# Kernel tuning notes

Measured on AMD Instinct MI355X. Metric: run time of the kernel, lower is better.

Reference implementation:

```python
import jax, jax.numpy as jnp
import numpy as np

N = 50000        # nodes
E = 500000       # edges
NUM = 4          # sampled intermediate neighbors per edge (self.num)
F = 64           # in_feats == out_feats (transform=False)
D = 32           # dist_dim
NB = 64          # embedding rows = len(boundaries)+1


def setup_inputs() -> dict:
    key = jax.random.key(0)
    ks = jax.random.split(key, 10)
    feat = jax.random.normal(ks[0], (N, F), jnp.float32)
    loc = jax.random.uniform(ks[1], (N, 3), jnp.float32)          # 3D positions in unit cube
    boundaries = jnp.sort(jax.random.uniform(ks[2], (NB - 1,), jnp.float32, 0.0, 2.0))
    embed_table = jax.random.normal(ks[3], (NB, D), jnp.float32)
    G_w = jax.random.normal(ks[4], (F, D), jnp.float32) / np.sqrt(D)      # Linear(dist_dim->out, no bias)
    agg_w = jax.random.normal(ks[5], (F, 2 * F), jnp.float32) / np.sqrt(2 * F)  # Linear(2*out->out)
    agg_b = jnp.zeros((F,), jnp.float32)
    src = jax.random.randint(ks[6], (E,), 0, N, jnp.int32)
    dst = jax.random.randint(ks[7], (E,), 0, N, jnp.int32)
    inter_ids = jax.random.randint(ks[8], (E, NUM), 0, N, jnp.int32)
    return dict(feat=feat, loc=loc, boundaries=boundaries, embed_table=embed_table,
                G_w=G_w, agg_w=agg_w, agg_b=agg_b, src=src, dst=dst, inter_ids=inter_ids)


def reference(feat, loc, boundaries, embed_table, G_w, agg_w, agg_b, src, dst, inter_ids):
    n = feat.shape[0]
    ones = jnp.ones((src.shape[0],), feat.dtype)
    # symmetric-ish degree normalization: d0 = in_deg^-0.5, d2 = out_deg^-0.5
    in_deg = jax.ops.segment_sum(ones, dst, num_segments=n)
    out_deg = jax.ops.segment_sum(ones, src, num_segments=n)
    d0 = jnp.clip(in_deg, 1.0) ** -0.5   # [N]
    d2 = jnp.clip(out_deg, 1.0) ** -0.5  # [N]

    # dist1 = ||loc[dst] - loc[src]||_2, bucketize -> embed -> G
    dist1 = jnp.linalg.norm(loc[dst] - loc[src], axis=1)              # [E]
    de1 = embed_table[jnp.searchsorted(boundaries, dist1)] @ G_w.T    # [E, F]

    # intermediate sampled neighbors: dist to each sampled node from edge src
    pos_src = loc[src]                                                # [E, 3]
    inter_pos = loc[inter_ids]                                        # [E, NUM, 3]
    dist_ = jnp.linalg.norm(pos_src[:, None, :] - inter_pos, axis=-1) # [E, NUM]
    de_ = embed_table[jnp.searchsorted(boundaries, dist_)] @ G_w.T    # [E, NUM, F]
    inter_h = feat[inter_ids]                                         # [E, NUM, F]
    dist_embed_dot_h = (de_ * inter_h).mean(axis=1)                   # [E, F]

    # h = d0[dst] * d2[src] * agg_fc([de1 * h_src, dist_embed_dot_h])
    cat = jnp.concatenate([de1 * feat[src], dist_embed_dot_h], axis=1)  # [E, 2F]
    msg = (d0[dst] * d2[src])[:, None] * (cat @ agg_w.T + agg_b)        # [E, F]

    # update_all(copy_e('h'), sum) -> scatter-sum messages to dst
    ft = jax.ops.segment_sum(msg, dst, num_segments=n)                  # [N, F]
    return ft
```

## Files before the change

### kernel.cpp

```cpp
#include <hip/hip_runtime.h>
#include <math.h>

#define LUTN 1024
#define LUTSCALE 512.0f
#define NBINS 50048
#define CHSH 12


__global__ __launch_bounds__(256) void prep_kernel(
    const float* __restrict__ embed, const float* __restrict__ G_w,
    const float* __restrict__ boundaries, const float* __restrict__ feat,
    const float* __restrict__ loc,
    float* __restrict__ M, int* __restrict__ lut,
    unsigned short* __restrict__ featH, float4* __restrict__ loc4, int N) {

    const int gid = blockIdx.x * 256 + threadIdx.x;
    const int gsz = gridDim.x * 256;
    for (int i = gid; i < 4096; i += gsz) {
        int b = i >> 6, f = i & 63;
        float acc = 0.f;
        #pragma unroll
        for (int dd = 0; dd < 32; ++dd) acc += embed[b * 32 + dd] * G_w[f * 32 + dd];
        M[i] = acc;
    }
    for (int i = gid; i < LUTN; i += gsz) {
        float left = (float)i * (1.0f / LUTSCALE);
        int c = 0;
        for (int j = 0; j < 63; ++j) c += (boundaries[j] < left) ? 1 : 0;
        lut[i] = c;
    }
    const int nq = N * 16;
    for (int i = gid; i < nq; i += gsz) {
        float4 v = ((const float4*)feat)[i];
        unsigned ux = __float_as_uint(v.x), uy = __float_as_uint(v.y);
        unsigned uz = __float_as_uint(v.z), uw = __float_as_uint(v.w);
        ushort4 h;
        h.x = (unsigned short)((ux + 0x7FFFu + ((ux >> 16) & 1u)) >> 16);
        h.y = (unsigned short)((uy + 0x7FFFu + ((uy >> 16) & 1u)) >> 16);
        h.z = (unsigned short)((uz + 0x7FFFu + ((uz >> 16) & 1u)) >> 16);
        h.w = (unsigned short)((uw + 0x7FFFu + ((uw >> 16) & 1u)) >> 16);
        ((ushort4*)featH)[i] = h;
    }
    for (int i = gid; i < N; i += gsz)
        loc4[i] = make_float4(loc[3 * i], loc[3 * i + 1], loc[3 * i + 2], 0.f);
}


__global__ __launch_bounds__(256) void hist_kernel(
    const int* __restrict__ src, const int* __restrict__ dst,
    unsigned char* __restrict__ pcnt, unsigned char* __restrict__ psrc,
    unsigned char* __restrict__ rnk8, int E) {

    __shared__ unsigned int hc[NBINS / 4];
    __shared__ unsigned int hs[NBINS / 4];
    for (int i = threadIdx.x; i < NBINS / 4; i += 256) { hc[i] = 0u; hs[i] = 0u; }
    __syncthreads();

    const int base = blockIdx.x << CHSH;
    const int lim  = min(E - base, 1 << CHSH);
    for (int t = threadIdx.x; t < lim; t += 256) {
        const int e = base + t;
        const int d = dst[e];
        const int s = src[e];
        const unsigned sh = (unsigned)(d & 3) * 8u;
        unsigned old = atomicAdd(&hc[d >> 2], 1u << sh);
        rnk8[e] = (unsigned char)((old >> sh) & 0xFFu);
        atomicAdd(&hs[s >> 2], 1u << ((unsigned)(s & 3) * 8u));
    }
    __syncthreads();

    unsigned int* gc = (unsigned int*)(pcnt + (size_t)blockIdx.x * NBINS);
    unsigned int* gs = (unsigned int*)(psrc + (size_t)blockIdx.x * NBINS);
    for (int i = threadIdx.x; i < NBINS / 4; i += 256) { gc[i] = hc[i]; gs[i] = hs[i]; }
}


__global__ __launch_bounds__(256) void merge_kernel(
    unsigned char* __restrict__ pcnt, const unsigned char* __restrict__ psrc,
    int* __restrict__ cnt, float* __restrict__ d2w, int P, int N) {

    const int d = blockIdx.x * 256 + threadIdx.x;
    if (d >= N) return;

    int sc = 0;
    #pragma unroll 4
    for (int p = 0; p < P; ++p) {
        const size_t idx = (size_t)p * NBINS + d;
        const int c = pcnt[idx];
        pcnt[idx] = (unsigned char)sc;
        sc += c;
    }
    cnt[d] = sc;

    int ss = 0;
    #pragma unroll 4
    for (int p = 0; p < P; ++p) ss += psrc[(size_t)p * NBINS + d];
    d2w[d] = rsqrtf(fmaxf((float)ss, 1.0f));
}


__global__ __launch_bounds__(1024) void scan_block_kernel(
    const int* __restrict__ cnt, int* __restrict__ startv,
    int* __restrict__ part, int N) {

    __shared__ int wsum[16];
    const int t = threadIdx.x, lane = t & 63, wv = t >> 6;
    const int i = blockIdx.x * 1024 + t;

    int v = (i < N) ? cnt[i] : 0;
    int x = v;
    #pragma unroll
    for (int off = 1; off < 64; off <<= 1) { int y = __shfl_up(x, off); if (lane >= off) x += y; }
    if (lane == 63) wsum[wv] = x;
    __syncthreads();
    if (t < 16) {
        int w = wsum[t], xx = w;
        #pragma unroll
        for (int off = 1; off < 16; off <<= 1) { int y = __shfl_up(xx, off); if (t >= off) xx += y; }
        wsum[t] = xx - w;
    }
    __syncthreads();
    int incl = x + wsum[wv];
    if (i < N) startv[i] = incl - v;
    if (t == 1023) part[blockIdx.x] = incl;
}

__device__ __forceinline__ void load_chunkoff(const int* __restrict__ part, int nb,
                                              int* __restrict__ co) {
    if (threadIdx.x < 64) {
        int v = (threadIdx.x < nb) ? part[threadIdx.x] : 0;
        int x = v;
        #pragma unroll
        for (int off = 1; off < 64; off <<= 1) {
            int y = __shfl_up(x, off);
            if ((threadIdx.x & 63) >= off) x += y;
        }
        co[threadIdx.x] = x - v;
    }
    __syncthreads();
}


__global__ __launch_bounds__(256) void edge_kernel(
    const float4* __restrict__ loc4, const float* __restrict__ boundaries,
    const int* __restrict__ lut,
    const int* __restrict__ src, const int* __restrict__ dst,
    const int* __restrict__ inter,
    const unsigned char* __restrict__ rnk8, const unsigned char* __restrict__ pcnt,
    const int* __restrict__ startv, const int* __restrict__ part,
    const float* __restrict__ d2w,
    int4* __restrict__ rec, int E, int nb) {

    __shared__ int lut_s[LUTN];
    __shared__ float bl[64];
    __shared__ int co[64];
    ((int4*)lut_s)[threadIdx.x] = ((const int4*)lut)[threadIdx.x];
    if (threadIdx.x < 64)
        bl[threadIdx.x] = (threadIdx.x < 63) ? boundaries[threadIdx.x] : 3.4e38f;
    load_chunkoff(part, nb, co);

    const int e = blockIdx.x * 256 + threadIdx.x;
    if (e >= E) return;

    const int s = src[e], d = dst[e];
    const int4 ii = ((const int4*)inter)[e];

    const float4 ps = loc4[s];
    float dist[5];
    {
        float4 pd = loc4[d];
        float dx = pd.x - ps.x, dy = pd.y - ps.y, dz = pd.z - ps.z;
        dist[0] = sqrtf(dx * dx + dy * dy + dz * dz);
    }
    const int id4[4] = {ii.x, ii.y, ii.z, ii.w};
    #pragma unroll
    for (int j = 0; j < 4; ++j) {
        float4 pt = loc4[id4[j]];
        float dx = pt.x - ps.x, dy = pt.y - ps.y, dz = pt.z - ps.z;
        dist[1 + j] = sqrtf(dx * dx + dy * dy + dz * dz);
    }
    unsigned pack = 0;
    #pragma unroll
    for (int q = 0; q < 5; ++q) {
        float dq = dist[q];
        int cell = (int)(dq * LUTSCALE);
        cell = (cell > LUTN - 1) ? (LUTN - 1) : cell;
        int b = lut_s[cell];
        while (b < 63 && bl[b] < dq) ++b;
        while (b > 0 && bl[b - 1] >= dq) --b;
        pack |= ((unsigned)b) << (6 * q);
    }

    const int p = e >> CHSH;
    const int cbase = pcnt[(size_t)p * NBINS + d];
    const int pos = startv[d] + co[d >> 10] + cbase + (int)rnk8[e];
    const float w = d2w[s];
    unsigned uw = __float_as_uint(w);
    unsigned wb = (uw + 0x7FFFu + ((uw >> 16) & 1u)) & 0xFFFF0000u;
    rec[pos] = make_int4(s | (ii.x << 16), ii.y | (ii.z << 16), ii.w | (int)wb, (int)pack);
}


__global__ __launch_bounds__(256) void node_kernel(
    const unsigned short* __restrict__ featH, const float* __restrict__ M,
    const int* __restrict__ cnt, const int* __restrict__ startv,
    const int* __restrict__ part, const int4* __restrict__ rec,
    float* __restrict__ cat, float* __restrict__ swb, int N, int nb) {

    __shared__ float Ms[4096];
    __shared__ int co[64];
    #pragma unroll
    for (int i = 0; i < 4; ++i)
        ((float4*)Ms)[threadIdx.x + 256 * i] = ((const float4*)M)[threadIdx.x + 256 * i];
    load_chunkoff(part, nb, co);

    const int lane = threadIdx.x & 63;
    const int wid  = threadIdx.x >> 6;
    const int d    = blockIdx.x * 4 + wid;
    if (d >= N) return;

    const int deg  = __builtin_amdgcn_readfirstlane(cnt[d]);
    const int base = __builtin_amdgcn_readfirstlane(startv[d] + co[d >> 10]);
    const int4* rp = rec + base;

    float acc0 = 0.f, acc1 = 0.f, sw = 0.f;

    #pragma unroll 4
    for (int k = 0; k < deg; ++k) {
        const int4 r = rp[k];
        const int s  = r.x & 0xFFFF;
        const int i0 = ((unsigned)r.x) >> 16;
        const int i1 = r.y & 0xFFFF;
        const int i2 = ((unsigned)r.y) >> 16;
        const int i3 = r.z & 0xFFFF;
        const float w = __uint_as_float((unsigned)r.z & 0xFFFF0000u);
        const unsigned pk = (unsigned)r.w;

        const float fs = __uint_as_float(((unsigned)featH[(size_t)s  * 64 + lane]) << 16);
        const float f0 = __uint_as_float(((unsigned)featH[(size_t)i0 * 64 + lane]) << 16);
        const float f1 = __uint_as_float(((unsigned)featH[(size_t)i1 * 64 + lane]) << 16);
        const float f2 = __uint_as_float(((unsigned)featH[(size_t)i2 * 64 + lane]) << 16);
        const float f3 = __uint_as_float(((unsigned)featH[(size_t)i3 * 64 + lane]) << 16);
        const float m0 = Ms[(pk & 63u) * 64 + lane];
        const float m1 = Ms[((pk >> 6) & 63u) * 64 + lane];
        const float m2 = Ms[((pk >> 12) & 63u) * 64 + lane];
        const float m3 = Ms[((pk >> 18) & 63u) * 64 + lane];
        const float m4 = Ms[((pk >> 24) & 63u) * 64 + lane];

        acc0 = fmaf(m0 * fs, w, acc0);
        float t = m1 * f0 + m2 * f1 + m3 * f2 + m4 * f3;
        acc1 = fmaf(0.25f * t, w, acc1);
        sw += w;
    }

    cat[(size_t)d * 128 + lane]      = acc0;
    cat[(size_t)d * 128 + 64 + lane] = acc1;
    if (lane == 0) swb[d] = sw;
}


__global__ __launch_bounds__(256) void epilogue_kernel(
    const float* __restrict__ cat, const float* __restrict__ agg_w,
    const float* __restrict__ agg_b, const float* __restrict__ swb,
    const int* __restrict__ cnt, float* __restrict__ out, int N) {

    const int lane = threadIdx.x & 63;
    const int wid  = threadIdx.x >> 6;

    float4 aw[32];
    const float4* awp = (const float4*)(agg_w + (size_t)lane * 128);
    #pragma unroll
    for (int i = 0; i < 32; ++i) aw[i] = awp[i];
    const float bias = agg_b[lane];

    const int gw = blockIdx.x * 4 + wid;
    const int stride = gridDim.x * 4;

    for (int d0i = gw; d0i < N; d0i += stride) {
        const int du = __builtin_amdgcn_readfirstlane(d0i);
        const float* cp = cat + (size_t)du * 128;
        float a0 = bias * swb[du], a1 = 0.f, a2 = 0.f, a3 = 0.f;
        #pragma unroll
        for (int k4 = 0; k4 < 32; k4 += 4) {
            float4 c0 = ((const float4*)cp)[k4];
            float4 c1 = ((const float4*)cp)[k4 + 1];
            float4 c2 = ((const float4*)cp)[k4 + 2];
            float4 c3 = ((const float4*)cp)[k4 + 3];
            a0 = fmaf(aw[k4].x, c0.x, a0); a0 = fmaf(aw[k4].y, c0.y, a0);
            a0 = fmaf(aw[k4].z, c0.z, a0); a0 = fmaf(aw[k4].w, c0.w, a0);
            a1 = fmaf(aw[k4+1].x, c1.x, a1); a1 = fmaf(aw[k4+1].y, c1.y, a1);
            a1 = fmaf(aw[k4+1].z, c1.z, a1); a1 = fmaf(aw[k4+1].w, c1.w, a1);
            a2 = fmaf(aw[k4+2].x, c2.x, a2); a2 = fmaf(aw[k4+2].y, c2.y, a2);
            a2 = fmaf(aw[k4+2].z, c2.z, a2); a2 = fmaf(aw[k4+2].w, c2.w, a2);
            a3 = fmaf(aw[k4+3].x, c3.x, a3); a3 = fmaf(aw[k4+3].y, c3.y, a3);
            a3 = fmaf(aw[k4+3].z, c3.z, a3); a3 = fmaf(aw[k4+3].w, c3.w, a3);
        }
        const float d0v = rsqrtf(fmaxf((float)cnt[du], 1.0f));
        out[(size_t)du * 64 + lane] = d0v * ((a0 + a1) + (a2 + a3));
    }
}


extern "C" void kernel_launch(void* const* d_in, const int* in_sizes, int n_in,
                              void* d_out, int out_size, void* d_ws, size_t ws_size,
                              hipStream_t stream) {
    const float* feat       = (const float*)d_in[0];
    const float* loc        = (const float*)d_in[1];
    const float* boundaries = (const float*)d_in[2];
    const float* embed      = (const float*)d_in[3];
    const float* G_w        = (const float*)d_in[4];
    const float* agg_w      = (const float*)d_in[5];
    const float* agg_b      = (const float*)d_in[6];
    const int*   src        = (const int*)d_in[7];
    const int*   dst        = (const int*)d_in[8];
    const int*   inter      = (const int*)d_in[9];

    const int N = in_sizes[0] / 64;
    const int E = in_sizes[7];

    const int P = (E + (1 << CHSH) - 1) >> CHSH;

    char* w = (char*)d_ws;
    auto take = [&](size_t bytes) { char* p = w; w += (bytes + 15) & ~(size_t)15; return p; };
    float*          M      = (float*)take(4096 * 4);
    int*            lut    = (int*)  take(LUTN * 4);
    int*            cnt    = (int*)  take((size_t)N * 4);
    int*            startv = (int*)  take((size_t)N * 4);
    int*            part   = (int*)  take(64 * 4);
    float*          d2w    = (float*)take((size_t)N * 4);
    int4*           rec    = (int4*) take((size_t)E * 16);
    unsigned char*  rnk8   = (unsigned char*)take((size_t)E);
    unsigned char*  pcnt   = (unsigned char*)take((size_t)P * NBINS);
    unsigned char*  psrc   = (unsigned char*)take((size_t)P * NBINS);
    float*          cat    = (float*)take((size_t)N * 128 * 4);
    float*          swb    = (float*)take((size_t)N * 4);
    unsigned short* featH  = (unsigned short*)take((size_t)N * 64 * 2);
    float4*         loc4   = (float4*)take((size_t)N * 16);
    float*          out    = (float*)d_out;

    const int eb = (E + 255) / 256;
    const int nb = (N + 1023) / 1024;
    const int mb = (N + 255) / 256;

    prep_kernel<<<1024, 256, 0, stream>>>(embed, G_w, boundaries, feat, loc,
                                          M, lut, featH, loc4, N);
    hist_kernel<<<P, 256, 0, stream>>>(src, dst, pcnt, psrc, rnk8, E);
    merge_kernel<<<mb, 256, 0, stream>>>(pcnt, psrc, cnt, d2w, P, N);
    scan_block_kernel<<<nb, 1024, 0, stream>>>(cnt, startv, part, N);
    edge_kernel<<<eb, 256, 0, stream>>>(loc4, boundaries, lut, src, dst, inter,
                                        rnk8, pcnt, startv, part, d2w, rec, E, nb);
    node_kernel<<<(N + 3) / 4, 256, 0, stream>>>(featH, M, cnt, startv, part, rec,
                                                 cat, swb, N, nb);
    epilogue_kernel<<<768, 256, 0, stream>>>(cat, agg_w, agg_b, swb, cnt, out, N);
}
```

Measured before the change: 232.9 us.

## Fuse prep/histogram and merge/scan kernels; split node gather across half-waves

The prep and histogram kernels become one launch, with histogram blocks and prep blocks running side by side. The histogram now reuses a single shared buffer for the dst and src passes, halving LDS so more blocks fit per CU. The merge and block-scan kernels are fused so counts feed the scan directly, removing a launch and a round trip of cnt. The node kernel now has each half-wave process alternate edges with 2-wide bf16 loads, then combines the halves with a cross-lane shuffle. This trades extra passes over src/dst and lower occupancy in merge_scan (1024-thread blocks) for fewer launches and more memory-level parallelism.

Measured after the change: 238.0 us. 2.2% more time.

```diff
diff --git a/kernel.cpp b/kernel.cpp
--- a/kernel.cpp
+++ b/kernel.cpp
@@ -4,18 +4,55 @@
 #define LUTN 1024
 #define LUTSCALE 512.0f
 #define NBINS 50048
+#define HCW (NBINS / 4)
 #define CHSH 12
 
 
-__global__ __launch_bounds__(256) void prep_kernel(
+__global__ __launch_bounds__(256) void front_kernel(
     const float* __restrict__ embed, const float* __restrict__ G_w,
     const float* __restrict__ boundaries, const float* __restrict__ feat,
     const float* __restrict__ loc,
+    const int* __restrict__ src, const int* __restrict__ dst,
     float* __restrict__ M, int* __restrict__ lut,
-    unsigned short* __restrict__ featH, float4* __restrict__ loc4, int N) {
-
-    const int gid = blockIdx.x * 256 + threadIdx.x;
-    const int gsz = gridDim.x * 256;
+    unsigned short* __restrict__ featH, float4* __restrict__ loc4,
+    unsigned char* __restrict__ pcnt, unsigned char* __restrict__ psrc,
+    unsigned char* __restrict__ rnk8,
+    int N, int E, int P, int PREPB) {
+
+    __shared__ unsigned int h[HCW];
+
+    if (blockIdx.x < P) {
+        const int base = blockIdx.x << CHSH;
+        const int lim  = min(E - base, 1 << CHSH);
+
+        for (int i = threadIdx.x; i < HCW; i += 256) h[i] = 0u;
+        __syncthreads();
+        for (int t = threadIdx.x; t < lim; t += 256) {
+            const int e = base + t;
+            const int dd = dst[e];
+            const unsigned sh = (unsigned)(dd & 3) * 8u;
+            unsigned old = atomicAdd(&h[dd >> 2], 1u << sh);
+            rnk8[e] = (unsigned char)((old >> sh) & 0xFFu);
+        }
+        __syncthreads();
+        unsigned int* gc = (unsigned int*)(pcnt + (size_t)blockIdx.x * NBINS);
+        for (int i = threadIdx.x; i < HCW; i += 256) gc[i] = h[i];
+        __syncthreads();
+
+        for (int i = threadIdx.x; i < HCW; i += 256) h[i] = 0u;
+        __syncthreads();
+        for (int t = threadIdx.x; t < lim; t += 256) {
+            const int s = src[base + t];
+            atomicAdd(&h[s >> 2], 1u << ((unsigned)(s & 3) * 8u));
+        }
+        __syncthreads();
+        unsigned int* gs = (unsigned int*)(psrc + (size_t)blockIdx.x * NBINS);
+        for (int i = threadIdx.x; i < HCW; i += 256) gs[i] = h[i];
+        return;
+    }
+
+    const int gid = (blockIdx.x - P) * 256 + threadIdx.x;
+    const int gsz = PREPB * 256;
     for (int i = gid; i < 4096; i += gsz) {
         int b = i >> 6, f = i & 63;
         float acc = 0.f;
@@ -34,80 +71,44 @@
         float4 v = ((const float4*)feat)[i];
         unsigned ux = __float_as_uint(v.x), uy = __float_as_uint(v.y);
         unsigned uz = __float_as_uint(v.z), uw = __float_as_uint(v.w);
-        ushort4 h;
-        h.x = (unsigned short)((ux + 0x7FFFu + ((ux >> 16) & 1u)) >> 16);
-        h.y = (unsigned short)((uy + 0x7FFFu + ((uy >> 16) & 1u)) >> 16);
-        h.z = (unsigned short)((uz + 0x7FFFu + ((uz >> 16) & 1u)) >> 16);
-        h.w = (unsigned short)((uw + 0x7FFFu + ((uw >> 16) & 1u)) >> 16);
-        ((ushort4*)featH)[i] = h;
+        ushort4 hh;
+        hh.x = (unsigned short)((ux + 0x7FFFu + ((ux >> 16) & 1u)) >> 16);
+        hh.y = (unsigned short)((uy + 0x7FFFu + ((uy >> 16) & 1u)) >> 16);
+        hh.z = (unsigned short)((uz + 0x7FFFu + ((uz >> 16) & 1u)) >> 16);
+        hh.w = (unsigned short)((uw + 0x7FFFu + ((uw >> 16) & 1u)) >> 16);
+        ((ushort4*)featH)[i] = hh;
     }
     for (int i = gid; i < N; i += gsz)
         loc4[i] = make_float4(loc[3 * i], loc[3 * i + 1], loc[3 * i + 2], 0.f);
 }
 
 
-__global__ __launch_bounds__(256) void hist_kernel(
-    const int* __restrict__ src, const int* __restrict__ dst,
-    unsigned char* __restrict__ pcnt, unsigned char* __restrict__ psrc,
-    unsigned char* __restrict__ rnk8, int E) {
-
-    __shared__ unsigned int hc[NBINS / 4];
-    __shared__ unsigned int hs[NBINS / 4];
-    for (int i = threadIdx.x; i < NBINS / 4; i += 256) { hc[i] = 0u; hs[i] = 0u; }
-    __syncthreads();
-
-    const int base = blockIdx.x << CHSH;
-    const int lim  = min(E - base, 1 << CHSH);
-    for (int t = threadIdx.x; t < lim; t += 256) {
-        const int e = base + t;
-        const int d = dst[e];
-        const int s = src[e];
-        const unsigned sh = (unsigned)(d & 3) * 8u;
-        unsigned old = atomicAdd(&hc[d >> 2], 1u << sh);
-        rnk8[e] = (unsigned char)((old >> sh) & 0xFFu);
-        atomicAdd(&hs[s >> 2], 1u << ((unsigned)(s & 3) * 8u));
-    }
-    __syncthreads();
-
-    unsigned int* gc = (unsigned int*)(pcnt + (size_t)blockIdx.x * NBINS);
-    unsigned int* gs = (unsigned int*)(psrc + (size_t)blockIdx.x * NBINS);
-    for (int i = threadIdx.x; i < NBINS / 4; i += 256) { gc[i] = hc[i]; gs[i] = hs[i]; }
-}
-
-
-__global__ __launch_bounds__(256) void merge_kernel(
+__global__ __launch_bounds__(1024) void merge_scan_kernel(
     unsigned char* __restrict__ pcnt, const unsigned char* __restrict__ psrc,
-    int* __restrict__ cnt, float* __restrict__ d2w, int P, int N) {
-
-    const int d = blockIdx.x * 256 + threadIdx.x;
-    if (d >= N) return;
-
-    int sc = 0;
-    #pragma unroll 4
-    for (int p = 0; p < P; ++p) {
-        const size_t idx = (size_t)p * NBINS + d;
-        const int c = pcnt[idx];
-        pcnt[idx] = (unsigned char)sc;
-        sc += c;
-    }
-    cnt[d] = sc;
-
-    int ss = 0;
-    #pragma unroll 4
-    for (int p = 0; p < P; ++p) ss += psrc[(size_t)p * NBINS + d];
-    d2w[d] = rsqrtf(fmaxf((float)ss, 1.0f));
-}
-
-
-__global__ __launch_bounds__(1024) void scan_block_kernel(
-    const int* __restrict__ cnt, int* __restrict__ startv,
-    int* __restrict__ part, int N) {
+    int* __restrict__ cnt, float* __restrict__ d2w,
+    int* __restrict__ startv, int* __restrict__ part, int P, int N) {
 
     __shared__ int wsum[16];
     const int t = threadIdx.x, lane = t & 63, wv = t >> 6;
-    const int i = blockIdx.x * 1024 + t;
-
-    int v = (i < N) ? cnt[i] : 0;
+    const int d = blockIdx.x * 1024 + t;
+
+    int sc = 0;
+    if (d < N) {
+        #pragma unroll 4
+        for (int p = 0; p < P; ++p) {
+            const size_t idx = (size_t)p * NBINS + d;
+            const int c = pcnt[idx];
+            pcnt[idx] = (unsigned char)sc;
+            sc += c;
+        }
+        cnt[d] = sc;
+        int ss = 0;
+        #pragma unroll 4
+        for (int p = 0; p < P; ++p) ss += psrc[(size_t)p * NBINS + d];
+        d2w[d] = rsqrtf(fmaxf((float)ss, 1.0f));
+    }
+
+    const int v = sc;
     int x = v;
     #pragma unroll
     for (int off = 1; off < 64; off <<= 1) { int y = __shfl_up(x, off); if (lane >= off) x += y; }
@@ -121,7 +122,7 @@
     }
     __syncthreads();
     int incl = x + wsum[wv];
-    if (i < N) startv[i] = incl - v;
+    if (d < N) startv[d] = incl - v;
     if (t == 1023) part[blockIdx.x] = incl;
 }
 
@@ -215,6 +216,8 @@
     load_chunkoff(part, nb, co);
 
     const int lane = threadIdx.x & 63;
+    const int h    = lane >> 5;
+    const int j    = lane & 31;
     const int wid  = threadIdx.x >> 6;
     const int d    = blockIdx.x * 4 + wid;
     if (d >= N) return;
@@ -223,11 +226,16 @@
     const int base = __builtin_amdgcn_readfirstlane(startv[d] + co[d >> 10]);
     const int4* rp = rec + base;
 
-    float acc0 = 0.f, acc1 = 0.f, sw = 0.f;
-
-    #pragma unroll 4
-    for (int k = 0; k < deg; ++k) {
-        const int4 r = rp[k];
+    float a0l = 0.f, a0h = 0.f, a1l = 0.f, a1h = 0.f, sw = 0.f;
+    const int kmax = (deg + 1) >> 1;
+
+    #pragma unroll 2
+    for (int k = 0; k < kmax; ++k) {
+        const int k2 = 2 * k + h;
+        int4 r;
+        if (k2 < deg) r = rp[k2];
+        else          r = make_int4(0, 0, 0, 0);
+
         const int s  = r.x & 0xFFFF;
         const int i0 = ((unsigned)r.x) >> 16;
         const int i1 = r.y & 0xFFFF;
@@ -236,26 +244,45 @@
         const float w = __uint_as_float((unsigned)r.z & 0xFFFF0000u);
         const unsigned pk = (unsigned)r.w;
 
-        const float fs = __uint_as_float(((unsigned)featH[(size_t)s  * 64 + lane]) << 16);
-        const float f0 = __uint_as_float(((unsigned)featH[(size_t)i0 * 64 + lane]) << 16);
-        const float f1 = __uint_as_float(((unsigned)featH[(size_t)i1 * 64 + lane]) << 16);
-        const float f2 = __uint_as_float(((unsigned)featH[(size_t)i2 * 64 + lane]) << 16);
-        const float f3 = __uint_as_float(((unsigned)featH[(size_t)i3 * 64 + lane]) << 16);
-        const float m0 = Ms[(pk & 63u) * 64 + lane];
-        const float m1 = Ms[((pk >> 6) & 63u) * 64 + lane];
-        const float m2 = Ms[((pk >> 12) & 63u) * 64 + lane];
-        const float m3 = Ms[((pk >> 18) & 63u) * 64 + lane];
-        const float m4 = Ms[((pk >> 24) & 63u) * 64 + lane];
-
-        acc0 = fmaf(m0 * fs, w, acc0);
-        float t = m1 * f0 + m2 * f1 + m3 * f2 + m4 * f3;
-        acc1 = fmaf(0.25f * t, w, acc1);
+        const unsigned fsu = *(const unsigned*)(featH + (size_t)s  * 64 + 2 * j);
+        const unsigned f0u = *(const unsigned*)(featH + (size_t)i0 * 64 + 2 * j);
+        const unsigned f1u = *(const unsigned*)(featH + (size_t)i1 * 64 + 2 * j);
+        const unsigned f2u = *(const unsigned*)(featH + (size_t)i2 * 64 + 2 * j);
+        const unsigned f3u = *(const unsigned*)(featH + (size_t)i3 * 64 + 2 * j);
+
+        const float2 m0 = *(const float2*)&Ms[(pk & 63u) * 64 + 2 * j];
+        const float2 m1 = *(const float2*)&Ms[((pk >> 6) & 63u) * 64 + 2 * j];
+        const float2 m2 = *(const float2*)&Ms[((pk >> 12) & 63u) * 64 + 2 * j];
+        const float2 m3 = *(const float2*)&Ms[((pk >> 18) & 63u) * 64 + 2 * j];
+        const float2 m4 = *(const float2*)&Ms[((pk >> 24) & 63u) * 64 + 2 * j];
+
+        const float fsl = __uint_as_float(fsu << 16), fsh = __uint_as_float(fsu & 0xFFFF0000u);
+        const float f0l = __uint_as_float(f0u << 16), f0h = __uint_as_float(f0u & 0xFFFF0000u);
+        const float f1l = __uint_as_float(f1u << 16), f1h = __uint_as_float(f1u & 0xFFFF0000u);
+        const float f2l = __uint_as_float(f2u << 16), f2h = __uint_as_float(f2u & 0xFFFF0000u);
+        const float f3l = __uint_as_float(f3u << 16), f3h = __uint_as_float(f3u & 0xFFFF0000u);
+
+        a0l = fmaf(m0.x * fsl, w, a0l);
+        a0h = fmaf(m0.y * fsh, w, a0h);
+        const float tl = m1.x * f0l + m2.x * f1l + m3.x * f2l + m4.x * f3l;
+        const float th = m1.y * f0h + m2.y * f1h + m3.y * f2h + m4.y * f3h;
+        a1l = fmaf(0.25f * tl, w, a1l);
+        a1h = fmaf(0.25f * th, w, a1h);
         sw += w;
     }
 
-    cat[(size_t)d * 128 + lane]      = acc0;
-    cat[(size_t)d * 128 + 64 + lane] = acc1;
-    if (lane == 0) swb[d] = sw;
+    const float b0l = __shfl_xor(a0l, 32, 64);
+    const float b0h = __shfl_xor(a0h, 32, 64);
+    const float b1l = __shfl_xor(a1l, 32, 64);
+    const float b1h = __shfl_xor(a1h, 32, 64);
+    const float swt = sw + __shfl_xor(sw, 32, 64);
+
+    if (h == 0) {
+        *(float2*)&cat[(size_t)d * 128 + 2 * j]      = make_float2(a0l + b0l, a0h + b0h);
+    } else {
+        *(float2*)&cat[(size_t)d * 128 + 64 + 2 * j] = make_float2(a1l + b1l, a1h + b1h);
+    }
+    if (lane == 0) swb[d] = swt;
 }
 
 
@@ -340,13 +367,12 @@
 
     const int eb = (E + 255) / 256;
     const int nb = (N + 1023) / 1024;
-    const int mb = (N + 255) / 256;
-
-    prep_kernel<<<1024, 256, 0, stream>>>(embed, G_w, boundaries, feat, loc,
-                                          M, lut, featH, loc4, N);
-    hist_kernel<<<P, 256, 0, stream>>>(src, dst, pcnt, psrc, rnk8, E);
-    merge_kernel<<<mb, 256, 0, stream>>>(pcnt, psrc, cnt, d2w, P, N);
-    scan_block_kernel<<<nb, 1024, 0, stream>>>(cnt, startv, part, N);
+    const int PREPB = 512;
+
+    front_kernel<<<P + PREPB, 256, 0, stream>>>(embed, G_w, boundaries, feat, loc,
+                                                src, dst, M, lut, featH, loc4,
+                                                pcnt, psrc, rnk8, N, E, P, PREPB);
+    merge_scan_kernel<<<nb, 1024, 0, stream>>>(pcnt, psrc, cnt, d2w, startv, part, P, N);
     edge_kernel<<<eb, 256, 0, stream>>>(loc4, boundaries, lut, src, dst, inter,
                                         rnk8, pcnt, startv, part, d2w, rec, E, nb);
     node_kernel<<<(N + 3) / 4, 256, 0, stream>>>(featH, M, cnt, startv, part, rec,
```

## Split node gather into two feature-half passes and fuse merge with scan

Applied to the files above, without the earlier changes.

Splits the bf16 feature table into two 32-column halves (featA/featB) and runs the node kernel twice, once per half. Each wave handles two edges at a time, one per 32-lane half, and combines the partial sums with a cross-lane shuffle. The aim is a smaller gather working set per pass (3.2 MB per half) so it fits better in cache, and to halve LDS use for the M table. It also fuses the merge and block-scan kernels into one launch to drop a kernel and the cnt round trip. The cost is that the edge records are read twice and there is one extra launch for the second node pass.

Result: slower. 272.0 us (+16.8%).

```diff
diff --git a/kernel.cpp b/kernel.cpp
--- a/kernel.cpp
+++ b/kernel.cpp
@@ -12,7 +12,8 @@
     const float* __restrict__ boundaries, const float* __restrict__ feat,
     const float* __restrict__ loc,
     float* __restrict__ M, int* __restrict__ lut,
-    unsigned short* __restrict__ featH, float4* __restrict__ loc4, int N) {
+    unsigned short* __restrict__ featA, unsigned short* __restrict__ featB,
+    float4* __restrict__ loc4, int N) {
 
     const int gid = blockIdx.x * 256 + threadIdx.x;
     const int gsz = gridDim.x * 256;
@@ -39,7 +40,9 @@
         h.y = (unsigned short)((uy + 0x7FFFu + ((uy >> 16) & 1u)) >> 16);
         h.z = (unsigned short)((uz + 0x7FFFu + ((uz >> 16) & 1u)) >> 16);
         h.w = (unsigned short)((uw + 0x7FFFu + ((uw >> 16) & 1u)) >> 16);
-        ((ushort4*)featH)[i] = h;
+        const int row = i >> 4, quad = i & 15;
+        if (quad < 8) ((ushort4*)featA)[row * 8 + quad]       = h;
+        else          ((ushort4*)featB)[row * 8 + (quad - 8)] = h;
     }
     for (int i = gid; i < N; i += gsz)
         loc4[i] = make_float4(loc[3 * i], loc[3 * i + 1], loc[3 * i + 2], 0.f);
@@ -75,39 +78,32 @@
 }
 
 
-__global__ __launch_bounds__(256) void merge_kernel(
+__global__ __launch_bounds__(1024) void merge_scan_kernel(
     unsigned char* __restrict__ pcnt, const unsigned char* __restrict__ psrc,
-    int* __restrict__ cnt, float* __restrict__ d2w, int P, int N) {
-
-    const int d = blockIdx.x * 256 + threadIdx.x;
-    if (d >= N) return;
-
-    int sc = 0;
-    #pragma unroll 4
-    for (int p = 0; p < P; ++p) {
-        const size_t idx = (size_t)p * NBINS + d;
-        const int c = pcnt[idx];
-        pcnt[idx] = (unsigned char)sc;
-        sc += c;
-    }
-    cnt[d] = sc;
-
-    int ss = 0;
-    #pragma unroll 4
-    for (int p = 0; p < P; ++p) ss += psrc[(size_t)p * NBINS + d];
-    d2w[d] = rsqrtf(fmaxf((float)ss, 1.0f));
-}
-
-
-__global__ __launch_bounds__(1024) void scan_block_kernel(
-    const int* __restrict__ cnt, int* __restrict__ startv,
-    int* __restrict__ part, int N) {
+    int* __restrict__ cnt, float* __restrict__ d2w,
+    int* __restrict__ startv, int* __restrict__ part, int P, int N) {
 
     __shared__ int wsum[16];
     const int t = threadIdx.x, lane = t & 63, wv = t >> 6;
-    const int i = blockIdx.x * 1024 + t;
-
-    int v = (i < N) ? cnt[i] : 0;
+    const int d = blockIdx.x * 1024 + t;
+
+    int sc = 0;
+    if (d < N) {
+        #pragma unroll 4
+        for (int p = 0; p < P; ++p) {
+            const size_t idx = (size_t)p * NBINS + d;
+            const int c = pcnt[idx];
+            pcnt[idx] = (unsigned char)sc;
+            sc += c;
+        }
+        cnt[d] = sc;
+        int ss = 0;
+        #pragma unroll 4
+        for (int p = 0; p < P; ++p) ss += psrc[(size_t)p * NBINS + d];
+        d2w[d] = rsqrtf(fmaxf((float)ss, 1.0f));
+    }
+
+    const int v = sc;
     int x = v;
     #pragma unroll
     for (int off = 1; off < 64; off <<= 1) { int y = __shfl_up(x, off); if (lane >= off) x += y; }
@@ -121,7 +117,7 @@
     }
     __syncthreads();
     int incl = x + wsum[wv];
-    if (i < N) startv[i] = incl - v;
+    if (d < N) startv[d] = incl - v;
     if (t == 1023) part[blockIdx.x] = incl;
 }
 
@@ -201,20 +197,21 @@
 }
 
 
-__global__ __launch_bounds__(256) void node_kernel(
-    const unsigned short* __restrict__ featH, const float* __restrict__ M,
+__global__ __launch_bounds__(256) void node_half_kernel(
+    const unsigned short* __restrict__ fH, const float* __restrict__ M,
     const int* __restrict__ cnt, const int* __restrict__ startv,
     const int* __restrict__ part, const int4* __restrict__ rec,
-    float* __restrict__ cat, float* __restrict__ swb, int N, int nb) {
-
-    __shared__ float Ms[4096];
+    float* __restrict__ cat, float* __restrict__ swb, int N, int nb, int pass) {
+
+    __shared__ float Ms[2048];
     __shared__ int co[64];
-    #pragma unroll
-    for (int i = 0; i < 4; ++i)
-        ((float4*)Ms)[threadIdx.x + 256 * i] = ((const float4*)M)[threadIdx.x + 256 * i];
+    for (int t = threadIdx.x; t < 2048; t += 256)
+        Ms[t] = M[(t >> 5) * 64 + (pass << 5) + (t & 31)];
     load_chunkoff(part, nb, co);
 
     const int lane = threadIdx.x & 63;
+    const int h    = lane >> 5;
+    const int j    = lane & 31;
     const int wid  = threadIdx.x >> 6;
     const int d    = blockIdx.x * 4 + wid;
     if (d >= N) return;
@@ -223,11 +220,16 @@
     const int base = __builtin_amdgcn_readfirstlane(startv[d] + co[d >> 10]);
     const int4* rp = rec + base;
 
-    float acc0 = 0.f, acc1 = 0.f, sw = 0.f;
-
-    #pragma unroll 4
-    for (int k = 0; k < deg; ++k) {
-        const int4 r = rp[k];
+    float a0 = 0.f, a1 = 0.f, sw = 0.f;
+    const int kmax = (deg + 1) >> 1;
+
+    #pragma unroll 2
+    for (int k = 0; k < kmax; ++k) {
+        const int k2 = 2 * k + h;
+        int4 r;
+        if (k2 < deg) r = rp[k2];
+        else          r = make_int4(0, 0, 0, 0);
+
         const int s  = r.x & 0xFFFF;
         const int i0 = ((unsigned)r.x) >> 16;
         const int i1 = r.y & 0xFFFF;
@@ -236,26 +238,30 @@
         const float w = __uint_as_float((unsigned)r.z & 0xFFFF0000u);
         const unsigned pk = (unsigned)r.w;
 
-        const float fs = __uint_as_float(((unsigned)featH[(size_t)s  * 64 + lane]) << 16);
-        const float f0 = __uint_as_float(((unsigned)featH[(size_t)i0 * 64 + lane]) << 16);
-        const float f1 = __uint_as_float(((unsigned)featH[(size_t)i1 * 64 + lane]) << 16);
-        const float f2 = __uint_as_float(((unsigned)featH[(size_t)i2 * 64 + lane]) << 16);
-        const float f3 = __uint_as_float(((unsigned)featH[(size_t)i3 * 64 + lane]) << 16);
-        const float m0 = Ms[(pk & 63u) * 64 + lane];
-        const float m1 = Ms[((pk >> 6) & 63u) * 64 + lane];
-        const float m2 = Ms[((pk >> 12) & 63u) * 64 + lane];
-        const float m3 = Ms[((pk >> 18) & 63u) * 64 + lane];
-        const float m4 = Ms[((pk >> 24) & 63u) * 64 + lane];
-
-        acc0 = fmaf(m0 * fs, w, acc0);
-        float t = m1 * f0 + m2 * f1 + m3 * f2 + m4 * f3;
-        acc1 = fmaf(0.25f * t, w, acc1);
+        const float fs = __uint_as_float(((unsigned)fH[(size_t)s  * 32 + j]) << 16);
+        const float f0 = __uint_as_float(((unsigned)fH[(size_t)i0 * 32 + j]) << 16);
+        const float f1 = __uint_as_float(((unsigned)fH[(size_t)i1 * 32 + j]) << 16);
+        const float f2 = __uint_as_float(((unsigned)fH[(size_t)i2 * 32 + j]) << 16);
+        const float f3 = __uint_as_float(((unsigned)fH[(size_t)i3 * 32 + j]) << 16);
+        const float m0 = Ms[(pk & 63u) * 32 + j];
+        const float m1 = Ms[((pk >> 6) & 63u) * 32 + j];
+        const float m2 = Ms[((pk >> 12) & 63u) * 32 + j];
+        const float m3 = Ms[((pk >> 18) & 63u) * 32 + j];
+        const float m4 = Ms[((pk >> 24) & 63u) * 32 + j];
+
+        a0 = fmaf(m0 * fs, w, a0);
+        const float t = m1 * f0 + m2 * f1 + m3 * f2 + m4 * f3;
+        a1 = fmaf(0.25f * t, w, a1);
         sw += w;
     }
 
-    cat[(size_t)d * 128 + lane]      = acc0;
-    cat[(size_t)d * 128 + 64 + lane] = acc1;
-    if (lane == 0) swb[d] = sw;
+    const float a0c = a0 + __shfl_xor(a0, 32, 64);
+    const float a1c = a1 + __shfl_xor(a1, 32, 64);
+    const float swt = sw + __shfl_xor(sw, 32, 64);
+
+    const int col = (pass << 5) + j;
+    cat[(size_t)d * 128 + (h ? 64 + col : col)] = h ? a1c : a0c;
+    if (pass == 0 && lane == 0) swb[d] = swt;
 }
 
 
@@ -334,22 +340,23 @@
     unsigned char*  psrc   = (unsigned char*)take((size_t)P * NBINS);
     float*          cat    = (float*)take((size_t)N * 128 * 4);
     float*          swb    = (float*)take((size_t)N * 4);
-    unsigned short* featH  = (unsigned short*)take((size_t)N * 64 * 2);
+    unsigned short* featA  = (unsigned short*)take((size_t)N * 32 * 2);
+    unsigned short* featB  = (unsigned short*)take((size_t)N * 32 * 2);
     float4*         loc4   = (float4*)take((size_t)N * 16);
     float*          out    = (float*)d_out;
 
     const int eb = (E + 255) / 256;
     const int nb = (N + 1023) / 1024;
-    const int mb = (N + 255) / 256;
 
     prep_kernel<<<1024, 256, 0, stream>>>(embed, G_w, boundaries, feat, loc,
-                                          M, lut, featH, loc4, N);
+                                          M, lut, featA, featB, loc4, N);
     hist_kernel<<<P, 256, 0, stream>>>(src, dst, pcnt, psrc, rnk8, E);
-    merge_kernel<<<mb, 256, 0, stream>>>(pcnt, psrc, cnt, d2w, P, N);
-    scan_block_kernel<<<nb, 1024, 0, stream>>>(cnt, startv, part, N);
+    merge_scan_kernel<<<nb, 1024, 0, stream>>>(pcnt, psrc, cnt, d2w, startv, part, P, N);
     edge_kernel<<<eb, 256, 0, stream>>>(loc4, boundaries, lut, src, dst, inter,
                                         rnk8, pcnt, startv, part, d2w, rec, E, nb);
-    node_kernel<<<(N + 3) / 4, 256, 0, stream>>>(featH, M, cnt, startv, part, rec,
-                                                 cat, swb, N, nb);
+    node_half_kernel<<<(N + 3) / 4, 256, 0, stream>>>(featA, M, cnt, startv, part, rec,
+                                                      cat, swb, N, nb, 0);
+    node_half_kernel<<<(N + 3) / 4, 256, 0, stream>>>(featB, M, cnt, startv, part, rec,
+                                                      cat, swb, N, nb, 1);
     epilogue_kernel<<<768, 256, 0, stream>>>(cat, agg_w, agg_b, swb, cnt, out, N);
 }
```

## Split histogram by role, fuse merge with scan, scalarize record fields

Applied to the files above, without the earlier changes.

The histogram kernel now runs two blocks per chunk, one counting dst and one counting src, each with a single shared-memory histogram and 512 threads. This halves LDS use per block and doubles block count for better occupancy. The merge and block-scan kernels are fused into one 1024-thread kernel, which removes a launch and a round trip through global memory for cnt. The node kernel reads the uniform edge-record fields through readfirstlane so index math stays in scalar registers. The fused merge has only 49 blocks, which may reduce parallelism for the strided per-partition reads.

After: 238.5 us. 1.02x slower.

```diff
diff --git a/kernel.cpp b/kernel.cpp
--- a/kernel.cpp
+++ b/kernel.cpp
@@ -46,68 +46,69 @@
 }
 
 
-__global__ __launch_bounds__(256) void hist_kernel(
+__global__ __launch_bounds__(512) void hist_kernel(
     const int* __restrict__ src, const int* __restrict__ dst,
     unsigned char* __restrict__ pcnt, unsigned char* __restrict__ psrc,
     unsigned char* __restrict__ rnk8, int E) {
 
-    __shared__ unsigned int hc[NBINS / 4];
-    __shared__ unsigned int hs[NBINS / 4];
-    for (int i = threadIdx.x; i < NBINS / 4; i += 256) { hc[i] = 0u; hs[i] = 0u; }
+    __shared__ unsigned int h[NBINS / 4];
+    for (int i = threadIdx.x; i < NBINS / 4; i += 512) h[i] = 0u;
     __syncthreads();
 
-    const int base = blockIdx.x << CHSH;
+    const int p    = blockIdx.x >> 1;
+    const int role = blockIdx.x & 1;
+    const int base = p << CHSH;
     const int lim  = min(E - base, 1 << CHSH);
-    for (int t = threadIdx.x; t < lim; t += 256) {
-        const int e = base + t;
-        const int d = dst[e];
-        const int s = src[e];
-        const unsigned sh = (unsigned)(d & 3) * 8u;
-        unsigned old = atomicAdd(&hc[d >> 2], 1u << sh);
-        rnk8[e] = (unsigned char)((old >> sh) & 0xFFu);
-        atomicAdd(&hs[s >> 2], 1u << ((unsigned)(s & 3) * 8u));
-    }
-    __syncthreads();
-
-    unsigned int* gc = (unsigned int*)(pcnt + (size_t)blockIdx.x * NBINS);
-    unsigned int* gs = (unsigned int*)(psrc + (size_t)blockIdx.x * NBINS);
-    for (int i = threadIdx.x; i < NBINS / 4; i += 256) { gc[i] = hc[i]; gs[i] = hs[i]; }
-}
-
-
-__global__ __launch_bounds__(256) void merge_kernel(
+
+    if (role == 0) {
+        for (int t = threadIdx.x; t < lim; t += 512) {
+            const int e = base + t;
+            const int d = dst[e];
+            const unsigned sh = (unsigned)(d & 3) * 8u;
+            unsigned old = atomicAdd(&h[d >> 2], 1u << sh);
+            rnk8[e] = (unsigned char)((old >> sh) & 0xFFu);
+        }
+        __syncthreads();
+        unsigned int* gc = (unsigned int*)(pcnt + (size_t)p * NBINS);
+        for (int i = threadIdx.x; i < NBINS / 4; i += 512) gc[i] = h[i];
+    } else {
+        for (int t = threadIdx.x; t < lim; t += 512) {
+            const int s = src[base + t];
+            atomicAdd(&h[s >> 2], 1u << ((unsigned)(s & 3) * 8u));
+        }
+        __syncthreads();
+        unsigned int* gs = (unsigned int*)(psrc + (size_t)p * NBINS);
+        for (int i = threadIdx.x; i < NBINS / 4; i += 512) gs[i] = h[i];
+    }
+}
+
+
+__global__ __launch_bounds__(1024) void merge_scan_kernel(
     unsigned char* __restrict__ pcnt, const unsigned char* __restrict__ psrc,
-    int* __restrict__ cnt, float* __restrict__ d2w, int P, int N) {
-
-    const int d = blockIdx.x * 256 + threadIdx.x;
-    if (d >= N) return;
-
-    int sc = 0;
-    #pragma unroll 4
-    for (int p = 0; p < P; ++p) {
-        const size_t idx = (size_t)p * NBINS + d;
-        const int c = pcnt[idx];
-        pcnt[idx] = (unsigned char)sc;
-        sc += c;
-    }
-    cnt[d] = sc;
-
-    int ss = 0;
-    #pragma unroll 4
-    for (int p = 0; p < P; ++p) ss += psrc[(size_t)p * NBINS + d];
-    d2w[d] = rsqrtf(fmaxf((float)ss, 1.0f));
-}
-
-
-__global__ __launch_bounds__(1024) void scan_block_kernel(
-    const int* __restrict__ cnt, int* __restrict__ startv,
-    int* __restrict__ part, int N) {
+    int* __restrict__ cnt, float* __restrict__ d2w,
+    int* __restrict__ startv, int* __restrict__ part, int P, int N) {
 
     __shared__ int wsum[16];
     const int t = threadIdx.x, lane = t & 63, wv = t >> 6;
-    const int i = blockIdx.x * 1024 + t;
-
-    int v = (i < N) ? cnt[i] : 0;
+    const int d = blockIdx.x * 1024 + t;
+
+    int sc = 0;
+    if (d < N) {
+        #pragma unroll 4
+        for (int p = 0; p < P; ++p) {
+            const size_t idx = (size_t)p * NBINS + d;
+            const int c = pcnt[idx];
+            pcnt[idx] = (unsigned char)sc;
+            sc += c;
+        }
+        cnt[d] = sc;
+        int ss = 0;
+        #pragma unroll 4
+        for (int p = 0; p < P; ++p) ss += psrc[(size_t)p * NBINS + d];
+        d2w[d] = rsqrtf(fmaxf((float)ss, 1.0f));
+    }
+
+    const int v = sc;
     int x = v;
     #pragma unroll
     for (int off = 1; off < 64; off <<= 1) { int y = __shfl_up(x, off); if (lane >= off) x += y; }
@@ -121,7 +122,7 @@
     }
     __syncthreads();
     int incl = x + wsum[wv];
-    if (i < N) startv[i] = incl - v;
+    if (d < N) startv[d] = incl - v;
     if (t == 1023) part[blockIdx.x] = incl;
 }
 
@@ -227,14 +228,19 @@
 
     #pragma unroll 4
     for (int k = 0; k < deg; ++k) {
-        const int4 r = rp[k];
-        const int s  = r.x & 0xFFFF;
-        const int i0 = ((unsigned)r.x) >> 16;
-        const int i1 = r.y & 0xFFFF;
-        const int i2 = ((unsigned)r.y) >> 16;
-        const int i3 = r.z & 0xFFFF;
-        const float w = __uint_as_float((unsigned)r.z & 0xFFFF0000u);
-        const unsigned pk = (unsigned)r.w;
+        const int4 rv = rp[k];
+        const int rx = __builtin_amdgcn_readfirstlane(rv.x);
+        const int ry = __builtin_amdgcn_readfirstlane(rv.y);
+        const int rz = __builtin_amdgcn_readfirstlane(rv.z);
+        const int rw = __builtin_amdgcn_readfirstlane(rv.w);
+
+        const int s  = rx & 0xFFFF;
+        const int i0 = ((unsigned)rx) >> 16;
+        const int i1 = ry & 0xFFFF;
+        const int i2 = ((unsigned)ry) >> 16;
+        const int i3 = rz & 0xFFFF;
+        const float w = __uint_as_float((unsigned)rz & 0xFFFF0000u);
+        const unsigned pk = (unsigned)rw;
 
         const float fs = __uint_as_float(((unsigned)featH[(size_t)s  * 64 + lane]) << 16);
         const float f0 = __uint_as_float(((unsigned)featH[(size_t)i0 * 64 + lane]) << 16);
@@ -340,13 +346,11 @@
 
     const int eb = (E + 255) / 256;
     const int nb = (N + 1023) / 1024;
-    const int mb = (N + 255) / 256;
 
     prep_kernel<<<1024, 256, 0, stream>>>(embed, G_w, boundaries, feat, loc,
                                           M, lut, featH, loc4, N);
-    hist_kernel<<<P, 256, 0, stream>>>(src, dst, pcnt, psrc, rnk8, E);
-    merge_kernel<<<mb, 256, 0, stream>>>(pcnt, psrc, cnt, d2w, P, N);
-    scan_block_kernel<<<nb, 1024, 0, stream>>>(cnt, startv, part, N);
+    hist_kernel<<<2 * P, 512, 0, stream>>>(src, dst, pcnt, psrc, rnk8, E);
+    merge_scan_kernel<<<nb, 1024, 0, stream>>>(pcnt, psrc, cnt, d2w, startv, part, P, N);
     edge_kernel<<<eb, 256, 0, stream>>>(loc4, boundaries, lut, src, dst, inter,
                                         rnk8, pcnt, startv, part, d2w, rec, E, nb);
     node_kernel<<<(N + 3) / 4, 256, 0, stream>>>(featH, M, cnt, startv, part, rec,
```
